# Kernel optimization log

Measured on AMD Instinct MI355X. Metric: run time of the kernel, lower is better.

The kernel has to match this reference:

```python
import jax, jax.numpy as jnp
import numpy as np

B, S, IN, OUT = 8, 4096, 1024, 1024


def setup_inputs() -> dict:
    key = jax.random.key(0)
    k1, k2, k3, k4, k5 = jax.random.split(key, 5)
    x = jax.random.normal(k1, (B, S, IN), dtype=jnp.float32)
    # pre-quantized int8 weight buffer [out, in]
    weight = jax.random.randint(k2, (OUT, IN), -127, 128, dtype=jnp.int32).astype(jnp.int8)
    bias = jax.random.normal(k3, (OUT,), dtype=jnp.float32) * 0.1
    # per-channel weight clip values (>0)
    w_clip_val = jax.random.uniform(k4, (OUT,), minval=0.5, maxval=2.0, dtype=jnp.float32)
    # smoothquant per-input-channel activation scaling factors (>0)
    smoothquant_scale = jax.random.uniform(k5, (IN,), minval=0.5, maxval=2.0, dtype=jnp.float32)
    return {"x": x, "weight": weight, "bias": bias,
            "w_clip_val": w_clip_val, "smoothquant_scale": smoothquant_scale}


def reference(x, weight, bias, w_clip_val, smoothquant_scale):
    # i8i8_aiu semantics for weight_quant_type='per_channel',
    # activ_quant_type='per_token' (symmetric -> zero_shift == 0), smoothquant=True.
    # 1) smoothquant: scale activations prior to quantization
    xs = x / smoothquant_scale                                   # [B,S,IN]
    # 2) per-token symmetric int8 quantization of activations
    a_scale = jnp.max(jnp.abs(xs), axis=-1, keepdims=True) / 127.0  # [B,S,1]
    a_scale = jnp.maximum(a_scale, 1e-8)
    x_int = jnp.round(jnp.clip(xs / a_scale, -127.0, 127.0)).astype(jnp.int8)
    acc = jax.lax.dot_general(x_int, weight,
                              dimension_numbers=(((2,), (1,)), ((), ())),
                              preferred_element_type=jnp.int32)
    # 4) fused dequant (per-token act scale * per-channel weight scale) + bias
    w_scale = w_clip_val / 127.0                                 # [OUT]
    return acc.astype(jnp.float32) * a_scale * w_scale + bias
```

## Files before the change

kernel.cpp:

```cpp
#include <hip/hip_runtime.h>
#include <stdint.h>

#define T_TOK 32768
#define NIN   1024
#define NOUT  1024
#define BM    64
#define NTHR  1024

typedef int v4i  __attribute__((ext_vector_type(4)));
typedef int v16i __attribute__((ext_vector_type(16)));

__global__ __launch_bounds__(256) void repack_w_frag(const int* __restrict__ w,
                                                     uint32_t* __restrict__ wf) {
  const int gid  = blockIdx.x * 256 + threadIdx.x;
  const int lane = gid & 63;
  const int ks   = (gid >> 6) & 31;
  const int nt   = gid >> 11;
  const int n    = nt * 32 + (lane & 31);
  const int kb   = ks * 32 + (lane >> 5) * 16;
  const int* src = w + (size_t)n * NIN + kb;
  uint32_t d[4];
#pragma unroll
  for (int q = 0; q < 4; ++q) {
    const int4 v = ((const int4*)src)[q];
    d[q] = (uint32_t)(v.x & 0xff) | ((uint32_t)(v.y & 0xff) << 8) |
           ((uint32_t)(v.z & 0xff) << 16) | ((uint32_t)(v.w & 0xff) << 24);
  }
  ((uint4*)wf)[gid] = make_uint4(d[0], d[1], d[2], d[3]);
}

__global__ __launch_bounds__(NTHR, 1) void fused_w8a8(
    const float* __restrict__ x,
    const uint8_t* __restrict__ wf,
    const float* __restrict__ sq,
    const float* __restrict__ wclip,
    const float* __restrict__ bias,
    float* __restrict__ asc_g,
    float* __restrict__ out)
{
  __shared__ __align__(16) uint8_t Af[BM * NIN];

  const int tid  = threadIdx.x;
  const int lane = tid & 63;
  const int w    = tid >> 6;
  const int t0   = blockIdx.x * BM;

  const uint8_t* wfw = wf + (((size_t)w * 2) * 32 * 64) * 16;
  auto ldB = [&](int ks, int j) -> v4i {
    return *(const v4i*)(wfw + ((((j * 32 + ks) * 64) + lane) << 4));
  };
  v4i Ba0 = ldB(0, 0), Ba1 = ldB(0, 1);
  v4i Bb0 = ldB(1, 0), Bb1 = ldB(1, 1);

  {
    const float4* sq4 = (const float4*)sq;
    float4 rs[4];
#pragma unroll
    for (int j = 0; j < 4; ++j) {
      const float4 s = sq4[j * 64 + lane];
      rs[j].x = __builtin_amdgcn_rcpf(s.x);
      rs[j].y = __builtin_amdgcn_rcpf(s.y);
      rs[j].z = __builtin_amdgcn_rcpf(s.z);
      rs[j].w = __builtin_amdgcn_rcpf(s.w);
    }
#pragma unroll
    for (int i = 0; i < 4; ++i) {
      const int tl = w * 4 + i;
      const float4* xr = (const float4*)(x + (size_t)(t0 + tl) * NIN);
      float4 v[4];
      float m = 0.f;
#pragma unroll
      for (int j = 0; j < 4; ++j) {
        float4 a = xr[j * 64 + lane];
        a.x *= rs[j].x; a.y *= rs[j].y; a.z *= rs[j].z; a.w *= rs[j].w;
        v[j] = a;
        m = fmaxf(m, fmaxf(fmaxf(fabsf(a.x), fabsf(a.y)),
                           fmaxf(fabsf(a.z), fabsf(a.w))));
      }
#pragma unroll
      for (int off = 1; off < 64; off <<= 1) m = fmaxf(m, __shfl_xor(m, off));
      const float as = fmaxf(m * (1.f / 127.f), 1e-8f);
      if (lane == 0) asc_g[t0 + tl] = as;
      const float ia = __builtin_amdgcn_rcpf(as);
      const int mt = tl >> 5;
#pragma unroll
      for (int j = 0; j < 4; ++j) {
        const int q0 = (int)rintf(fminf(fmaxf(v[j].x * ia, -127.f), 127.f));
        const int q1 = (int)rintf(fminf(fmaxf(v[j].y * ia, -127.f), 127.f));
        const int q2 = (int)rintf(fminf(fmaxf(v[j].z * ia, -127.f), 127.f));
        const int q3 = (int)rintf(fminf(fmaxf(v[j].w * ia, -127.f), 127.f));
        const uint32_t d = (uint32_t)(q0 & 0xff) | ((uint32_t)(q1 & 0xff) << 8) |
                           ((uint32_t)(q2 & 0xff) << 16) | ((uint32_t)(q3 & 0xff) << 24);
        const int di  = j * 64 + lane;
        const int ksw = di >> 3;
        const int h   = (di >> 2) & 1;
        const int slot = (tl & 31) + 32 * h;
        const int chunk = (mt * 32 + ksw) * 64 + (slot ^ (ksw & 7));
        *(uint32_t*)(Af + chunk * 16 + (di & 3) * 4) = d;
      }
    }
  }
  __syncthreads();

  auto ldA = [&](int mt, int ks) -> v4i {
    return *(const v4i*)(Af + ((((mt * 32 + ks) * 64) + (lane ^ (ks & 7))) << 4));
  };

  v16i acc00 = {}, acc01 = {}, acc10 = {}, acc11 = {};

  for (int ks = 0; ks < 32; ks += 2) {
    {
      const v4i a0 = ldA(0, ks), a1 = ldA(1, ks);
      __builtin_amdgcn_s_setprio(1);
      acc00 = __builtin_amdgcn_mfma_i32_32x32x32_i8(a0, Ba0, acc00, 0, 0, 0);
      acc01 = __builtin_amdgcn_mfma_i32_32x32x32_i8(a0, Ba1, acc01, 0, 0, 0);
      acc10 = __builtin_amdgcn_mfma_i32_32x32x32_i8(a1, Ba0, acc10, 0, 0, 0);
      acc11 = __builtin_amdgcn_mfma_i32_32x32x32_i8(a1, Ba1, acc11, 0, 0, 0);
      __builtin_amdgcn_s_setprio(0);
      if (ks + 2 < 32) { Ba0 = ldB(ks + 2, 0); Ba1 = ldB(ks + 2, 1); }
    }
    {
      const v4i a0 = ldA(0, ks + 1), a1 = ldA(1, ks + 1);
      __builtin_amdgcn_s_setprio(1);
      acc00 = __builtin_amdgcn_mfma_i32_32x32x32_i8(a0, Bb0, acc00, 0, 0, 0);
      acc01 = __builtin_amdgcn_mfma_i32_32x32x32_i8(a0, Bb1, acc01, 0, 0, 0);
      acc10 = __builtin_amdgcn_mfma_i32_32x32x32_i8(a1, Bb0, acc10, 0, 0, 0);
      acc11 = __builtin_amdgcn_mfma_i32_32x32x32_i8(a1, Bb1, acc11, 0, 0, 0);
      __builtin_amdgcn_s_setprio(0);
      if (ks + 3 < 32) { Bb0 = ldB(ks + 3, 0); Bb1 = ldB(ks + 3, 1); }
    }
  }

  const int hr = 4 * (lane >> 5);
  const float* ascw = asc_g + t0;

#define EPI(ACC, MT, NTL)                                                    \
  do {                                                                       \
    const int n = w * 64 + (NTL) * 32 + (lane & 31);                         \
    const float wsc = wclip[n] * (1.f / 127.f);                              \
    const float bs  = bias[n];                                               \
    _Pragma("unroll")                                                        \
    for (int reg = 0; reg < 16; ++reg) {                                     \
      const int r = (MT) * 32 + (reg & 3) + 8 * (reg >> 2) + hr;             \
      out[(size_t)(t0 + r) * NOUT + n] =                                     \
          (float)ACC[reg] * ascw[r] * wsc + bs;                              \
    }                                                                        \
  } while (0)

  EPI(acc00, 0, 0);
  EPI(acc01, 0, 1);
  EPI(acc10, 1, 0);
  EPI(acc11, 1, 1);
#undef EPI
}

extern "C" void kernel_launch(void* const* d_in, const int* in_sizes, int n_in,
                              void* d_out, int out_size, void* d_ws, size_t ws_size,
                              hipStream_t stream) {
  const float* x      = (const float*)d_in[0];
  const int*   weight = (const int*)d_in[1];
  const float* bias   = (const float*)d_in[2];
  const float* wclip  = (const float*)d_in[3];
  const float* sq     = (const float*)d_in[4];
  float* out = (float*)d_out;

  uint32_t* wfrag = (uint32_t*)d_ws;
  float*    asc_g = (float*)((uint8_t*)d_ws + (size_t)(NOUT / 32) * 32 * 64 * 16);

  repack_w_frag<<<(NOUT * NIN / 16) / 256, 256, 0, stream>>>(weight, wfrag);
  fused_w8a8<<<T_TOK / BM, NTHR, 0, stream>>>(x, (const uint8_t*)wfrag,
                                              sq, wclip, bias, asc_g, out);
}
```

Before: 80.05 us.

## Halve token tile, widen per-wave N tile, keep scales in LDS

Shrinks the token tile from 64 to 32 rows and the block from 1024 to 512 threads, with each of 8 waves now covering 128 output columns (4 N-fragments sharing one A fragment) instead of 64. The per-token activation scales move from a global workspace into shared memory. x loads and output stores become nontemporal, and the weight-fragment prefetch is issued after quantization rather than before. The aim is higher occupancy (4 blocks per CU with 32KB LDS), fewer LDS A reads per MFMA, and less cache pollution from streaming data. The cost is more B-fragment registers per wave and twice the total weight reads from L2 across blocks.

```diff
diff --git a/kernel.cpp b/kernel.cpp
--- a/kernel.cpp
+++ b/kernel.cpp
@@ -4,11 +4,14 @@
 #define T_TOK 32768
 #define NIN   1024
 #define NOUT  1024
-#define BM    64
-#define NTHR  1024
+#define BM    32
+#define NTHR  512
 
-typedef int v4i  __attribute__((ext_vector_type(4)));
-typedef int v16i __attribute__((ext_vector_type(16)));
+typedef int   v4i  __attribute__((ext_vector_type(4)));
+typedef int   v16i __attribute__((ext_vector_type(16)));
+typedef float v4f  __attribute__((ext_vector_type(4)));
+
+#define MFMA_I8(a, b, c) __builtin_amdgcn_mfma_i32_32x32x32_i8(a, b, c, 0, 0, 0)
 
 __global__ __launch_bounds__(256) void repack_w_frag(const int* __restrict__ w,
                                                      uint32_t* __restrict__ wf) {
@@ -29,35 +32,28 @@
   ((uint4*)wf)[gid] = make_uint4(d[0], d[1], d[2], d[3]);
 }
 
-__global__ __launch_bounds__(NTHR, 1) void fused_w8a8(
+__global__ __launch_bounds__(NTHR, 4) void fused_w8a8(
     const float* __restrict__ x,
     const uint8_t* __restrict__ wf,
     const float* __restrict__ sq,
     const float* __restrict__ wclip,
     const float* __restrict__ bias,
-    float* __restrict__ asc_g,
     float* __restrict__ out)
 {
   __shared__ __align__(16) uint8_t Af[BM * NIN];
+  __shared__ float ascale_s[BM];
 
   const int tid  = threadIdx.x;
   const int lane = tid & 63;
   const int w    = tid >> 6;
   const int t0   = blockIdx.x * BM;
 
-  const uint8_t* wfw = wf + (((size_t)w * 2) * 32 * 64) * 16;
-  auto ldB = [&](int ks, int j) -> v4i {
-    return *(const v4i*)(wfw + ((((j * 32 + ks) * 64) + lane) << 4));
-  };
-  v4i Ba0 = ldB(0, 0), Ba1 = ldB(0, 1);
-  v4i Bb0 = ldB(1, 0), Bb1 = ldB(1, 1);
-
   {
-    const float4* sq4 = (const float4*)sq;
-    float4 rs[4];
+    const v4f* sq4 = (const v4f*)sq;
+    v4f rs[4];
 #pragma unroll
     for (int j = 0; j < 4; ++j) {
-      const float4 s = sq4[j * 64 + lane];
+      const v4f s = sq4[j * 64 + lane];
       rs[j].x = __builtin_amdgcn_rcpf(s.x);
       rs[j].y = __builtin_amdgcn_rcpf(s.y);
       rs[j].z = __builtin_amdgcn_rcpf(s.z);
@@ -66,12 +62,12 @@
 #pragma unroll
     for (int i = 0; i < 4; ++i) {
       const int tl = w * 4 + i;
-      const float4* xr = (const float4*)(x + (size_t)(t0 + tl) * NIN);
-      float4 v[4];
+      const v4f* xr = (const v4f*)(x + (size_t)(t0 + tl) * NIN);
+      v4f v[4];
       float m = 0.f;
 #pragma unroll
       for (int j = 0; j < 4; ++j) {
-        float4 a = xr[j * 64 + lane];
+        v4f a = __builtin_nontemporal_load(&xr[j * 64 + lane]);
         a.x *= rs[j].x; a.y *= rs[j].y; a.z *= rs[j].z; a.w *= rs[j].w;
         v[j] = a;
         m = fmaxf(m, fmaxf(fmaxf(fabsf(a.x), fabsf(a.y)),
@@ -80,9 +76,8 @@
 #pragma unroll
       for (int off = 1; off < 64; off <<= 1) m = fmaxf(m, __shfl_xor(m, off));
       const float as = fmaxf(m * (1.f / 127.f), 1e-8f);
-      if (lane == 0) asc_g[t0 + tl] = as;
+      if (lane == 0) ascale_s[tl] = as;
       const float ia = __builtin_amdgcn_rcpf(as);
-      const int mt = tl >> 5;
 #pragma unroll
       for (int j = 0; j < 4; ++j) {
         const int q0 = (int)rintf(fminf(fmaxf(v[j].x * ia, -127.f), 127.f));
@@ -91,66 +86,83 @@
         const int q3 = (int)rintf(fminf(fmaxf(v[j].w * ia, -127.f), 127.f));
         const uint32_t d = (uint32_t)(q0 & 0xff) | ((uint32_t)(q1 & 0xff) << 8) |
                            ((uint32_t)(q2 & 0xff) << 16) | ((uint32_t)(q3 & 0xff) << 24);
-        const int di  = j * 64 + lane;
-        const int ksw = di >> 3;
-        const int h   = (di >> 2) & 1;
-        const int slot = (tl & 31) + 32 * h;
-        const int chunk = (mt * 32 + ksw) * 64 + (slot ^ (ksw & 7));
-        *(uint32_t*)(Af + chunk * 16 + (di & 3) * 4) = d;
+        const int di   = j * 64 + lane;
+        const int ksw  = di >> 3;
+        const int h    = (di >> 2) & 1;
+        const int slot = ((tl ^ (ksw & 7)) & 31) + 32 * h;
+        *(uint32_t*)(&Af[(ksw * 64 + slot) * 16 + (di & 3) * 4]) = d;
       }
     }
   }
+
+  const uint8_t* wfw = wf + ((size_t)(w * 4) << 15);
+  auto ldB = [&](int ks, int j) -> v4i {
+    return *(const v4i*)(wfw + ((((j * 32 + ks) * 64) + lane) << 4));
+  };
+  v4i Ba0 = ldB(0, 0), Ba1 = ldB(0, 1), Ba2 = ldB(0, 2), Ba3 = ldB(0, 3);
+  v4i Bb0 = ldB(1, 0), Bb1 = ldB(1, 1), Bb2 = ldB(1, 2), Bb3 = ldB(1, 3);
+
   __syncthreads();
 
-  auto ldA = [&](int mt, int ks) -> v4i {
-    return *(const v4i*)(Af + ((((mt * 32 + ks) * 64) + (lane ^ (ks & 7))) << 4));
+  auto ldA = [&](int ks) -> v4i {
+    return *(const v4i*)(&Af[((ks * 64) + (lane ^ (ks & 7))) << 4]);
   };
 
-  v16i acc00 = {}, acc01 = {}, acc10 = {}, acc11 = {};
+  v16i acc0 = {}, acc1 = {}, acc2 = {}, acc3 = {};
 
   for (int ks = 0; ks < 32; ks += 2) {
     {
-      const v4i a0 = ldA(0, ks), a1 = ldA(1, ks);
+      const v4i a = ldA(ks);
       __builtin_amdgcn_s_setprio(1);
-      acc00 = __builtin_amdgcn_mfma_i32_32x32x32_i8(a0, Ba0, acc00, 0, 0, 0);
-      acc01 = __builtin_amdgcn_mfma_i32_32x32x32_i8(a0, Ba1, acc01, 0, 0, 0);
-      acc10 = __builtin_amdgcn_mfma_i32_32x32x32_i8(a1, Ba0, acc10, 0, 0, 0);
-      acc11 = __builtin_amdgcn_mfma_i32_32x32x32_i8(a1, Ba1, acc11, 0, 0, 0);
+      acc0 = MFMA_I8(a, Ba0, acc0);
+      acc1 = MFMA_I8(a, Ba1, acc1);
+      acc2 = MFMA_I8(a, Ba2, acc2);
+      acc3 = MFMA_I8(a, Ba3, acc3);
       __builtin_amdgcn_s_setprio(0);
-      if (ks + 2 < 32) { Ba0 = ldB(ks + 2, 0); Ba1 = ldB(ks + 2, 1); }
+      if (ks + 2 < 32) {
+        Ba0 = ldB(ks + 2, 0); Ba1 = ldB(ks + 2, 1);
+        Ba2 = ldB(ks + 2, 2); Ba3 = ldB(ks + 2, 3);
+      }
     }
     {
-      const v4i a0 = ldA(0, ks + 1), a1 = ldA(1, ks + 1);
+      const v4i a = ldA(ks + 1);
       __builtin_amdgcn_s_setprio(1);
-      acc00 = __builtin_amdgcn_mfma_i32_32x32x32_i8(a0, Bb0, acc00, 0, 0, 0);
-      acc01 = __builtin_amdgcn_mfma_i32_32x32x32_i8(a0, Bb1, acc01, 0, 0, 0);
-      acc10 = __builtin_amdgcn_mfma_i32_32x32x32_i8(a1, Bb0, acc10, 0, 0, 0);
-      acc11 = __builtin_amdgcn_mfma_i32_32x32x32_i8(a1, Bb1, acc11, 0, 0, 0);
+      acc0 = MFMA_I8(a, Bb0, acc0);
+      acc1 = MFMA_I8(a, Bb1, acc1);
+      acc2 = MFMA_I8(a, Bb2, acc2);
+      acc3 = MFMA_I8(a, Bb3, acc3);
       __builtin_amdgcn_s_setprio(0);
-      if (ks + 3 < 32) { Bb0 = ldB(ks + 3, 0); Bb1 = ldB(ks + 3, 1); }
+      if (ks + 3 < 32) {
+        Bb0 = ldB(ks + 3, 0); Bb1 = ldB(ks + 3, 1);
+        Bb2 = ldB(ks + 3, 2); Bb3 = ldB(ks + 3, 3);
+      }
     }
   }
 
   const int hr = 4 * (lane >> 5);
-  const float* ascw = asc_g + t0;
+  float ascv[16];
+#pragma unroll
+  for (int reg = 0; reg < 16; ++reg)
+    ascv[reg] = ascale_s[(reg & 3) + 8 * (reg >> 2) + hr];
 
-#define EPI(ACC, MT, NTL)                                                    \
+#define EPI(ACC, NTL)                                                        \
   do {                                                                       \
-    const int n = w * 64 + (NTL) * 32 + (lane & 31);                         \
+    const int n = w * 128 + (NTL) * 32 + (lane & 31);                        \
     const float wsc = wclip[n] * (1.f / 127.f);                              \
     const float bs  = bias[n];                                               \
     _Pragma("unroll")                                                        \
     for (int reg = 0; reg < 16; ++reg) {                                     \
-      const int r = (MT) * 32 + (reg & 3) + 8 * (reg >> 2) + hr;             \
-      out[(size_t)(t0 + r) * NOUT + n] =                                     \
-          (float)ACC[reg] * ascw[r] * wsc + bs;                              \
+      const int r = (reg & 3) + 8 * (reg >> 2) + hr;                         \
+      __builtin_nontemporal_store(                                           \
+          (float)ACC[reg] * ascv[reg] * wsc + bs,                            \
+          &out[(size_t)(t0 + r) * NOUT + n]);                                \
     }                                                                        \
   } while (0)
 
-  EPI(acc00, 0, 0);
-  EPI(acc01, 0, 1);
-  EPI(acc10, 1, 0);
-  EPI(acc11, 1, 1);
+  EPI(acc0, 0);
+  EPI(acc1, 1);
+  EPI(acc2, 2);
+  EPI(acc3, 3);
 #undef EPI
 }
 
@@ -165,9 +177,8 @@
   float* out = (float*)d_out;
 
   uint32_t* wfrag = (uint32_t*)d_ws;
-  float*    asc_g = (float*)((uint8_t*)d_ws + (size_t)(NOUT / 32) * 32 * 64 * 16);
 
   repack_w_frag<<<(NOUT * NIN / 16) / 256, 256, 0, stream>>>(weight, wfrag);
   fused_w8a8<<<T_TOK / BM, NTHR, 0, stream>>>(x, (const uint8_t*)wfrag,
-                                              sq, wclip, bias, asc_g, out);
+                                              sq, wclip, bias, out);
 }
```

Result: slower. 91.45 us (+14.2%).
